# Kernel optimization log

Measured on AMD Instinct MI355X. Metric: run time of the kernel, lower is better.

## Reference

```python
import jax, jax.numpy as jnp
import numpy as np

B, NC, CN, K, DN = 2, 256, 256, 16, 64
G, HM, HS, HMOD, MOD_OUT = 8, 128, 128, 64, 5


def setup_inputs() -> dict:
    rng = np.random.default_rng(0)
    # per-neuron top-K neighbors within cell, excluding self, sorted (matches torch buffer build)
    scores = rng.random((NC, CN, CN)).astype(np.float32)
    ii = np.arange(CN)
    scores[:, ii, ii] = -np.inf
    conn = np.argpartition(-scores, K, axis=-1)[..., :K]
    conn = np.sort(conn, axis=-1).astype(np.int32)  # [NC, CN, K]

    key = jax.random.key(0)
    ks = jax.random.split(key, 12)
    n = lambda k, s, sc=1.0: jax.random.normal(k, s, jnp.float32) * sc
    return {
        'h': n(ks[0], (B, NC, CN, DN), 0.01),
        'w_conn': n(ks[1], (B, NC, CN, K), 0.1),
        'cell_context': n(ks[2], (B, NC, DN), 0.1),
        'neuron_id': n(ks[3], (NC, CN, DN), 0.02),
        'msg_w1': n(ks[4], (G, HM, 3 * DN), 0.05), 'msg_b1': jnp.zeros((G, HM)),
        'msg_w2': n(ks[5], (G, DN, HM), 0.005), 'msg_b2': jnp.zeros((G, DN)),
        'state_w1': n(ks[6], (G, HS, 3 * DN), 0.05), 'state_b1': jnp.zeros((G, HS)),
        'state_w2': n(ks[7], (G, DN, HS), 0.005), 'state_b2': jnp.zeros((G, DN)),
        'mod_w1': n(ks[8], (NC, 2 * DN, HMOD), 0.05), 'mod_b1': jnp.zeros((NC, HMOD)),
        'mod_w2': n(ks[9], (NC, HMOD, MOD_OUT), 0.0005), 'mod_b2': jnp.zeros((NC, MOD_OUT)),
        'conn_idx': jnp.asarray(conn),
        'cell_to_group': (jnp.arange(NC) % G).astype(jnp.int32),
    }


def reference(h, w_conn, cell_context, neuron_id,
              msg_w1, msg_b1, msg_w2, msg_b2,
              state_w1, state_b1, state_w2, state_b2,
              mod_w1, mod_b1, mod_w2, mod_b2,
              conn_idx, cell_to_group):
    nc = h.shape[1]
    cell_ix = jnp.arange(nc)[:, None, None]
    # gather K-neighbor states per neuron: [B, NC, CN, K, DN]
    nb = jax.vmap(lambda hb: hb[cell_ix, conn_idx])(h)
    # connection-weighted aggregation
    agg = jnp.einsum('bnck,bnckd->bncd', w_conn, nb)

    g = cell_to_group  # [NC]
    # grouped message MLP (2-layer), per-cell weights gathered from group table
    mfeat = jnp.concatenate([h, agg, jnp.broadcast_to(neuron_id[None], h.shape)], axis=-1)
    mh = jax.nn.gelu(jnp.einsum('bncf,nhf->bnch', mfeat, msg_w1[g]) + msg_b1[g][None, :, None, :])
    msg = jnp.einsum('bnch,ndh->bncd', mh, msg_w2[g]) + msg_b2[g][None, :, None, :]

    # grouped state MLP, residual update on h
    ctx = jnp.broadcast_to(cell_context[:, :, None, :], h.shape)
    sfeat = jnp.concatenate([h, msg, ctx], axis=-1)
    sh = jax.nn.gelu(jnp.einsum('bncf,nhf->bnch', sfeat, state_w1[g]) + state_b1[g][None, :, None, :])
    h_new = h + jnp.einsum('bnch,ndh->bncd', sh, state_w2[g]) + state_b2[g][None, :, None, :]

    # per-cell modulation MLP on pooled stats (h_mean || msg_mean)
    pooled = jnp.concatenate([h_new.mean(axis=2), msg.mean(axis=2)], axis=-1)  # [B, NC, 2DN]
    ph = jax.nn.gelu(jnp.einsum('bnf,nfh->bnh', pooled, mod_w1) + mod_b1[None])
    mod = jnp.einsum('bnh,nho->bno', ph, mod_w2) + mod_b2[None]
    return h_new, msg, mod
```

## Files before the change

### kernel.cpp

```cpp
#include <hip/hip_runtime.h>

#define B_   2
#define NC_  256
#define CN_  256
#define K_   16
#define DN_  64
#define G_   8
#define HM_  128
#define F3_  192

typedef unsigned short u16;
typedef short v8s __attribute__((ext_vector_type(8)));
typedef float v4f __attribute__((ext_vector_type(4)));

#define SMEM_BYTES 158336


__device__ __forceinline__ u16 f2b(float f) {
    unsigned v; __builtin_memcpy(&v, &f, 4);
    v = v + 0x7fffu + ((v >> 16) & 1u);
    return (u16)(v >> 16);
}
__device__ __forceinline__ v8s cvt8(const float* p) {
    float4 a = *(const float4*)p, b = *(const float4*)(p + 4);
    v8s r;
    r[0] = (short)f2b(a.x); r[1] = (short)f2b(a.y); r[2] = (short)f2b(a.z); r[3] = (short)f2b(a.w);
    r[4] = (short)f2b(b.x); r[5] = (short)f2b(b.y); r[6] = (short)f2b(b.z); r[7] = (short)f2b(b.w);
    return r;
}
__device__ __forceinline__ float gelu_t(float x) {
    float u = x * x;
    float t = 1.5957691216057308f * x * __builtin_fmaf(0.044715f, u, 1.0f);
    float e = __expf(-t);
    return x * __builtin_amdgcn_rcpf(1.0f + e);
}

__global__ __launch_bounds__(256) void cvt_w(
    const float* __restrict__ mw1, const float* __restrict__ mw2,
    const float* __restrict__ sw1, const float* __restrict__ sw2,
    u16* __restrict__ dst)
{
    int e = (blockIdx.x * 256 + threadIdx.x) * 4;
    const float* s; int off;
    if      (e < 196608) { s = mw1; off = e; }
    else if (e < 262144) { s = mw2; off = e - 196608; }
    else if (e < 458752) { s = sw1; off = e - 262144; }
    else                 { s = sw2; off = e - 458752; }
    float4 v = *(const float4*)(s + off);
    ushort4 o4;
    o4.x = f2b(v.x); o4.y = f2b(v.y); o4.z = f2b(v.z); o4.w = f2b(v.w);
    *(ushort4*)(dst + e) = o4;
}

__global__ __launch_bounds__(512) void mg_main(
    const float* __restrict__ h,    const float* __restrict__ wconn,
    const float* __restrict__ ctx,  const float* __restrict__ nid,
    const u16* __restrict__ mw1b,   const float* __restrict__ mb1,
    const u16* __restrict__ mw2b,   const float* __restrict__ mb2,
    const u16* __restrict__ sw1b,   const float* __restrict__ sb1,
    const u16* __restrict__ sw2b,   const float* __restrict__ sb2,
    const int* __restrict__ conn,   const int* __restrict__ c2g,
    const float* __restrict__ dw1,  const float* __restrict__ db1,
    const float* __restrict__ dw2,  const float* __restrict__ db2,
    float* __restrict__ outf)
{
    const int bn   = blockIdx.x;
    const int n    = bn & 255;
    const int tid  = threadIdx.x;
    const int wave = tid >> 6;
    const int lane = tid & 63;
    const int q    = lane >> 4;
    const int ln   = lane & 15;
    const int g    = c2g[n];

    extern __shared__ char smem[];
    u16*   hT   = (u16*)(smem);
    u16*   big  = (u16*)(smem + 34816);
    u16*   am   = (u16*)(smem + 104448);
    u16*   ctxl = (u16*)(smem + 141312);
    float* hsum = (float*)(smem + 141440);
    float* msum = (float*)(smem + 149632);
    float* pool = (float*)(smem + 157824);

    const size_t hbase = (size_t)bn * (CN_ * DN_);
    const size_t nbase = (size_t)n  * (CN_ * DN_);
    float* oH = outf + (size_t)bn * 16384;
    float* oM = outf + (size_t)8388608 + (size_t)bn * 16384;

    if (tid < 64) ctxl[tid] = f2b(ctx[(size_t)bn * DN_ + tid]);
    {
        const int row  = tid & 255;
        const int half = tid >> 8;
        const float* hrow = h + hbase + (size_t)row * DN_ + half * 32;
#pragma unroll
        for (int i = 0; i < 8; ++i) {
            float4 v = *(const float4*)(hrow + i * 4);
            int d0 = half * 32 + i * 4;
            hT[(d0 + 0) * 272 + row] = f2b(v.x);
            hT[(d0 + 1) * 272 + row] = f2b(v.y);
            hT[(d0 + 2) * 272 + row] = f2b(v.z);
            hT[(d0 + 3) * 272 + row] = f2b(v.w);
        }
    }
    __syncthreads();

    {
        const int sg   = wave >> 2;
        const int wl   = wave & 3;
        const int gtid = tid & 255;
        u16* wgg = (u16*)(smem + 34816 + sg * 34816);

        for (int s = 0; s < 4; s += 2) {
            const int st = s + sg;
#pragma unroll
            for (int i = 0; i < 9; ++i) {
                int idx = gtid + i * 256;
                if (idx < 2176) ((uint4*)wgg)[idx] = make_uint4(0u, 0u, 0u, 0u);
            }
            __syncthreads();
#pragma unroll
            for (int i = 0; i < 4; ++i) {
                int p  = i * 256 + gtid;
                int cl = p >> 4;
                int iv = conn[n * 4096 + st * 1024 + p];
                float wv = wconn[(size_t)bn * 4096 + st * 1024 + p];
                wgg[cl * 272 + iv] = f2b(wv);
            }
            __syncthreads();
            {
                v4f a0 = {0,0,0,0}, a1 = {0,0,0,0}, a2 = {0,0,0,0}, a3 = {0,0,0,0};
                const u16* arow = wgg + (wl * 16 + ln) * 272 + q * 8;
#pragma unroll
                for (int ks = 0; ks < 8; ++ks) {
                    v8s a   = *(const v8s*)(arow + ks * 32);
                    v8s bb0 = *(const v8s*)(hT + ( 0 + ln) * 272 + ks * 32 + q * 8);
                    v8s bb1 = *(const v8s*)(hT + (16 + ln) * 272 + ks * 32 + q * 8);
                    v8s bb2 = *(const v8s*)(hT + (32 + ln) * 272 + ks * 32 + q * 8);
                    v8s bb3 = *(const v8s*)(hT + (48 + ln) * 272 + ks * 32 + q * 8);
                    a0 = __builtin_amdgcn_mfma_f32_16x16x32_bf16(a, bb0, a0, 0, 0, 0);
                    a1 = __builtin_amdgcn_mfma_f32_16x16x32_bf16(a, bb1, a1, 0, 0, 0);
                    a2 = __builtin_amdgcn_mfma_f32_16x16x32_bf16(a, bb2, a2, 0, 0, 0);
                    a3 = __builtin_amdgcn_mfma_f32_16x16x32_bf16(a, bb3, a3, 0, 0, 0);
                }
                int crow = st * 64 + wl * 16 + q * 4;
#pragma unroll
                for (int r = 0; r < 4; ++r) {
                    am[(crow + r) * 72 +  0 + ln] = f2b(a0[r]);
                    am[(crow + r) * 72 + 16 + ln] = f2b(a1[r]);
                    am[(crow + r) * 72 + 32 + ln] = f2b(a2[r]);
                    am[(crow + r) * 72 + 48 + ln] = f2b(a3[r]);
                }
            }
            __syncthreads();
        }
    }

    const int cbase = wave * 32;

    {
        v8s afr[2][6];
#pragma unroll
        for (int mi = 0; mi < 2; ++mi) {
            int c = cbase + mi * 16 + ln;
            afr[mi][0] = cvt8(h + hbase + (size_t)c * 64 +  0 + q * 8);
            afr[mi][1] = cvt8(h + hbase + (size_t)c * 64 + 32 + q * 8);
            afr[mi][2] = *(const v8s*)(am + c * 72 +  0 + q * 8);
            afr[mi][3] = *(const v8s*)(am + c * 72 + 32 + q * 8);
            afr[mi][4] = cvt8(nid + nbase + (size_t)c * 64 +  0 + q * 8);
            afr[mi][5] = cvt8(nid + nbase + (size_t)c * 64 + 32 + q * 8);
        }
        float b1v[8];
#pragma unroll
        for (int nt = 0; nt < 8; ++nt) b1v[nt] = mb1[g * HM_ + nt * 16 + ln];
        const u16* w1g = mw1b + (size_t)g * HM_ * F3_;
#pragma unroll
        for (int nt = 0; nt < 8; ++nt) {
            v4f acc[2] = {{0,0,0,0},{0,0,0,0}};
#pragma unroll
            for (int ks = 0; ks < 6; ++ks) {
                v8s bf = *(const v8s*)(w1g + (nt * 16 + ln) * F3_ + ks * 32 + q * 8);
#pragma unroll
                for (int mi = 0; mi < 2; ++mi)
                    acc[mi] = __builtin_amdgcn_mfma_f32_16x16x32_bf16(afr[mi][ks], bf, acc[mi], 0, 0, 0);
            }
#pragma unroll
            for (int mi = 0; mi < 2; ++mi) {
                int c = cbase + mi * 16 + q * 4;
#pragma unroll
                for (int r = 0; r < 4; ++r)
                    big[(c + r) * 136 + nt * 16 + ln] = f2b(gelu_t(acc[mi][r] + b1v[nt]));
            }
        }
    }

    {
        v8s afr[2][4];
#pragma unroll
        for (int mi = 0; mi < 2; ++mi) {
            int c = cbase + mi * 16 + ln;
#pragma unroll
            for (int ks = 0; ks < 4; ++ks)
                afr[mi][ks] = *(const v8s*)(big + c * 136 + ks * 32 + q * 8);
        }
        const u16* w2g = mw2b + (size_t)g * DN_ * HM_;
        float mpart[4];
#pragma unroll
        for (int nt = 0; nt < 4; ++nt) {
            float bb = mb2[g * DN_ + nt * 16 + ln];
            v4f acc[2] = {{0,0,0,0},{0,0,0,0}};
#pragma unroll
            for (int ks = 0; ks < 4; ++ks) {
                v8s bf = *(const v8s*)(w2g + (nt * 16 + ln) * HM_ + ks * 32 + q * 8);
#pragma unroll
                for (int mi = 0; mi < 2; ++mi)
                    acc[mi] = __builtin_amdgcn_mfma_f32_16x16x32_bf16(afr[mi][ks], bf, acc[mi], 0, 0, 0);
            }
            float ms = 0.0f;
            int d = nt * 16 + ln;
#pragma unroll
            for (int mi = 0; mi < 2; ++mi) {
                int c = cbase + mi * 16 + q * 4;
#pragma unroll
                for (int r = 0; r < 4; ++r) {
                    float mv = acc[mi][r] + bb;
                    am[(c + r) * 72 + d] = f2b(mv);
                    oM[(size_t)(c + r) * 64 + d] = mv;
                    ms += mv;
                }
            }
            mpart[nt] = ms;
        }
#pragma unroll
        for (int nt = 0; nt < 4; ++nt)
            msum[(wave * 4 + q) * 64 + nt * 16 + ln] = mpart[nt];
    }

    {
        v8s cfr0 = *(const v8s*)(ctxl +  0 + q * 8);
        v8s cfr1 = *(const v8s*)(ctxl + 32 + q * 8);
        v8s afr[2][4];
#pragma unroll
        for (int mi = 0; mi < 2; ++mi) {
            int c = cbase + mi * 16 + ln;
            afr[mi][0] = cvt8(h + hbase + (size_t)c * 64 +  0 + q * 8);
            afr[mi][1] = cvt8(h + hbase + (size_t)c * 64 + 32 + q * 8);
            afr[mi][2] = *(const v8s*)(am + c * 72 +  0 + q * 8);
            afr[mi][3] = *(const v8s*)(am + c * 72 + 32 + q * 8);
        }
        float b1v[8];
#pragma unroll
        for (int nt = 0; nt < 8; ++nt) b1v[nt] = sb1[g * HM_ + nt * 16 + ln];
        const u16* w1g = sw1b + (size_t)g * HM_ * F3_;
#pragma unroll
        for (int nt = 0; nt < 8; ++nt) {
            v4f acc[2] = {{0,0,0,0},{0,0,0,0}};
#pragma unroll
            for (int ks = 0; ks < 4; ++ks) {
                v8s bf = *(const v8s*)(w1g + (nt * 16 + ln) * F3_ + ks * 32 + q * 8);
#pragma unroll
                for (int mi = 0; mi < 2; ++mi)
                    acc[mi] = __builtin_amdgcn_mfma_f32_16x16x32_bf16(afr[mi][ks], bf, acc[mi], 0, 0, 0);
            }
#pragma unroll
            for (int ks = 4; ks < 6; ++ks) {
                v8s bf = *(const v8s*)(w1g + (nt * 16 + ln) * F3_ + ks * 32 + q * 8);
                v8s aa = (ks == 4) ? cfr0 : cfr1;
#pragma unroll
                for (int mi = 0; mi < 2; ++mi)
                    acc[mi] = __builtin_amdgcn_mfma_f32_16x16x32_bf16(aa, bf, acc[mi], 0, 0, 0);
            }
#pragma unroll
            for (int mi = 0; mi < 2; ++mi) {
                int c = cbase + mi * 16 + q * 4;
#pragma unroll
                for (int r = 0; r < 4; ++r)
                    big[(c + r) * 136 + nt * 16 + ln] = f2b(gelu_t(acc[mi][r] + b1v[nt]));
            }
        }
    }

    {
        v8s afr[2][4];
#pragma unroll
        for (int mi = 0; mi < 2; ++mi) {
            int c = cbase + mi * 16 + ln;
#pragma unroll
            for (int ks = 0; ks < 4; ++ks)
                afr[mi][ks] = *(const v8s*)(big + c * 136 + ks * 32 + q * 8);
        }
        const u16* w2g = sw2b + (size_t)g * DN_ * HM_;
        float hpart[4];
#pragma unroll
        for (int nt = 0; nt < 4; ++nt) {
            float bb = sb2[g * DN_ + nt * 16 + ln];
            v4f acc[2] = {{0,0,0,0},{0,0,0,0}};
#pragma unroll
            for (int ks = 0; ks < 4; ++ks) {
                v8s bf = *(const v8s*)(w2g + (nt * 16 + ln) * HM_ + ks * 32 + q * 8);
#pragma unroll
                for (int mi = 0; mi < 2; ++mi)
                    acc[mi] = __builtin_amdgcn_mfma_f32_16x16x32_bf16(afr[mi][ks], bf, acc[mi], 0, 0, 0);
            }
            float hs = 0.0f;
            int d = nt * 16 + ln;
#pragma unroll
            for (int mi = 0; mi < 2; ++mi) {
                int c = cbase + mi * 16 + q * 4;
#pragma unroll
                for (int r = 0; r < 4; ++r) {
                    float hv = h[hbase + (size_t)(c + r) * 64 + d];
                    float hn = hv + acc[mi][r] + bb;
                    oH[(size_t)(c + r) * 64 + d] = hn;
                    hs += hn;
                }
            }
            hpart[nt] = hs;
        }
#pragma unroll
        for (int nt = 0; nt < 4; ++nt)
            hsum[(wave * 4 + q) * 64 + nt * 16 + ln] = hpart[nt];
    }
    __syncthreads();

    if (tid < 128) {
        int col = tid & 63;
        const float* src = (tid < 64) ? hsum : msum;
        float s = 0.0f;
#pragma unroll
        for (int i = 0; i < 32; ++i) s += src[i * 64 + col];
        pool[tid] = s * (1.0f / 256.0f);
    }
    __syncthreads();

    {
        const int col = tid & 63, fh = tid >> 6;
        const float* w1p = dw1 + ((size_t)n * 128 + fh * 16) * 64 + col;
        const float* pv  = pool + fh * 16;
        float acc = 0.0f;
#pragma unroll
        for (int f = 0; f < 16; ++f)
            acc = __builtin_fmaf(pv[f], w1p[(size_t)f * 64], acc);
        hsum[fh * 64 + col] = acc;
    }
    __syncthreads();

    if (tid < 64) {
        float a = db1[n * 64 + tid];
#pragma unroll
        for (int j = 0; j < 8; ++j) a += hsum[j * 64 + tid];
        float ph = gelu_t(a);
        float part[5];
#pragma unroll
        for (int o = 0; o < 5; ++o) part[o] = ph * dw2[((size_t)n * 64 + tid) * 5 + o];
#pragma unroll
        for (int off = 32; off > 0; off >>= 1)
#pragma unroll
            for (int o = 0; o < 5; ++o) part[o] += __shfl_down(part[o], off);
        if (tid == 0) {
#pragma unroll
            for (int o = 0; o < 5; ++o)
                outf[(size_t)16777216 + bn * 5 + o] = part[o] + db2[n * 5 + o];
        }
    }
}

extern "C" void kernel_launch(void* const* d_in, const int* in_sizes, int n_in,
                              void* d_out, int out_size, void* d_ws, size_t ws_size,
                              hipStream_t stream) {
    const float* h     = (const float*)d_in[0];
    const float* wconn = (const float*)d_in[1];
    const float* ctx   = (const float*)d_in[2];
    const float* nid   = (const float*)d_in[3];
    const float* mw1   = (const float*)d_in[4];
    const float* mb1   = (const float*)d_in[5];
    const float* mw2   = (const float*)d_in[6];
    const float* mb2   = (const float*)d_in[7];
    const float* sw1   = (const float*)d_in[8];
    const float* sb1   = (const float*)d_in[9];
    const float* sw2   = (const float*)d_in[10];
    const float* sb2   = (const float*)d_in[11];
    const float* dw1   = (const float*)d_in[12];
    const float* db1   = (const float*)d_in[13];
    const float* dw2   = (const float*)d_in[14];
    const float* db2   = (const float*)d_in[15];
    const int* conn    = (const int*)d_in[16];
    const int* c2g     = (const int*)d_in[17];
    float* outf  = (float*)d_out;
    u16*   wb    = (u16*)d_ws;

    hipFuncSetAttribute(reinterpret_cast<const void*>(&mg_main),
                        hipFuncAttributeMaxDynamicSharedMemorySize, SMEM_BYTES);

    cvt_w<<<512, 256, 0, stream>>>(mw1, mw2, sw1, sw2, wb);
    mg_main<<<512, 512, SMEM_BYTES, stream>>>(h, wconn, ctx, nid,
                                              wb,           mb1,
                                              wb + 196608,  mb2,
                                              wb + 262144,  sb1,
                                              wb + 458752,  sb2,
                                              conn, c2g,
                                              dw1, db1, dw2, db2,
                                              outf);
}
```

Baseline: 235.5 us.

## Split each cell across two blocks and gather neighbors directly instead of via MFMA

The main kernel now launches 1024 blocks of 256 threads, each covering half of a cell's neurons, with much smaller LDS so that two blocks fit per CU. The neighbor aggregation no longer builds a dense 256x256 scatter matrix for an MFMA. Instead each wave gathers bf16 h rows with readlane-broadcast indices and weights and accumulates with scalar FMAs. h is converted to bf16 once in LDS and reused for the MLP inputs. Pooled partial means go to workspace, and a new small kernel runs the modulation MLP, which adds a launch and a global round trip.

```diff
diff --git a/kernel.cpp b/kernel.cpp
--- a/kernel.cpp
+++ b/kernel.cpp
@@ -13,7 +13,7 @@
 typedef short v8s __attribute__((ext_vector_type(8)));
 typedef float v4f __attribute__((ext_vector_type(4)));
 
-#define SMEM_BYTES 158336
+#define SMEM_BYTES 63616
 
 
 __device__ __forceinline__ u16 f2b(float f) {
@@ -52,7 +52,7 @@
     *(ushort4*)(dst + e) = o4;
 }
 
-__global__ __launch_bounds__(512) void mg_main(
+__global__ __launch_bounds__(256, 2) void mg_main(
     const float* __restrict__ h,    const float* __restrict__ wconn,
     const float* __restrict__ ctx,  const float* __restrict__ nid,
     const u16* __restrict__ mw1b,   const float* __restrict__ mb1,
@@ -60,12 +60,13 @@
     const u16* __restrict__ sw1b,   const float* __restrict__ sb1,
     const u16* __restrict__ sw2b,   const float* __restrict__ sb2,
     const int* __restrict__ conn,   const int* __restrict__ c2g,
-    const float* __restrict__ dw1,  const float* __restrict__ db1,
-    const float* __restrict__ dw2,  const float* __restrict__ db2,
-    float* __restrict__ outf)
+    float* __restrict__ outf,       float* __restrict__ partial)
 {
-    const int bn   = blockIdx.x;
-    const int n    = bn & 255;
+    const int bx   = blockIdx.x;
+    const int bnc  = bx & 511;
+    const int half = bx >> 9;
+    const int r0   = half * 128;
+    const int n    = bnc & 255;
     const int tid  = threadIdx.x;
     const int wave = tid >> 6;
     const int lane = tid & 63;
@@ -74,133 +75,98 @@
     const int g    = c2g[n];
 
     extern __shared__ char smem[];
-    u16*   hT   = (u16*)(smem);
-    u16*   big  = (u16*)(smem + 34816);
-    u16*   am   = (u16*)(smem + 104448);
-    u16*   ctxl = (u16*)(smem + 141312);
-    float* hsum = (float*)(smem + 141440);
-    float* msum = (float*)(smem + 149632);
-    float* pool = (float*)(smem + 157824);
-
-    const size_t hbase = (size_t)bn * (CN_ * DN_);
-    const size_t nbase = (size_t)n  * (CN_ * DN_);
-    float* oH = outf + (size_t)bn * 16384;
-    float* oM = outf + (size_t)8388608 + (size_t)bn * 16384;
-
-    if (tid < 64) ctxl[tid] = f2b(ctx[(size_t)bn * DN_ + tid]);
-    {
-        const int row  = tid & 255;
-        const int half = tid >> 8;
-        const float* hrow = h + hbase + (size_t)row * DN_ + half * 32;
-#pragma unroll
-        for (int i = 0; i < 8; ++i) {
-            float4 v = *(const float4*)(hrow + i * 4);
-            int d0 = half * 32 + i * 4;
-            hT[(d0 + 0) * 272 + row] = f2b(v.x);
-            hT[(d0 + 1) * 272 + row] = f2b(v.y);
-            hT[(d0 + 2) * 272 + row] = f2b(v.z);
-            hT[(d0 + 3) * 272 + row] = f2b(v.w);
-        }
-    }
-    __syncthreads();
-
-    {
-        const int sg   = wave >> 2;
-        const int wl   = wave & 3;
-        const int gtid = tid & 255;
-        u16* wgg = (u16*)(smem + 34816 + sg * 34816);
-
-        for (int s = 0; s < 4; s += 2) {
-            const int st = s + sg;
-#pragma unroll
-            for (int i = 0; i < 9; ++i) {
-                int idx = gtid + i * 256;
-                if (idx < 2176) ((uint4*)wgg)[idx] = make_uint4(0u, 0u, 0u, 0u);
-            }
-            __syncthreads();
-#pragma unroll
-            for (int i = 0; i < 4; ++i) {
-                int p  = i * 256 + gtid;
-                int cl = p >> 4;
-                int iv = conn[n * 4096 + st * 1024 + p];
-                float wv = wconn[(size_t)bn * 4096 + st * 1024 + p];
-                wgg[cl * 272 + iv] = f2b(wv);
-            }
-            __syncthreads();
-            {
-                v4f a0 = {0,0,0,0}, a1 = {0,0,0,0}, a2 = {0,0,0,0}, a3 = {0,0,0,0};
-                const u16* arow = wgg + (wl * 16 + ln) * 272 + q * 8;
-#pragma unroll
-                for (int ks = 0; ks < 8; ++ks) {
-                    v8s a   = *(const v8s*)(arow + ks * 32);
-                    v8s bb0 = *(const v8s*)(hT + ( 0 + ln) * 272 + ks * 32 + q * 8);
-                    v8s bb1 = *(const v8s*)(hT + (16 + ln) * 272 + ks * 32 + q * 8);
-                    v8s bb2 = *(const v8s*)(hT + (32 + ln) * 272 + ks * 32 + q * 8);
-                    v8s bb3 = *(const v8s*)(hT + (48 + ln) * 272 + ks * 32 + q * 8);
-                    a0 = __builtin_amdgcn_mfma_f32_16x16x32_bf16(a, bb0, a0, 0, 0, 0);
-                    a1 = __builtin_amdgcn_mfma_f32_16x16x32_bf16(a, bb1, a1, 0, 0, 0);
-                    a2 = __builtin_amdgcn_mfma_f32_16x16x32_bf16(a, bb2, a2, 0, 0, 0);
-                    a3 = __builtin_amdgcn_mfma_f32_16x16x32_bf16(a, bb3, a3, 0, 0, 0);
-                }
-                int crow = st * 64 + wl * 16 + q * 4;
-#pragma unroll
-                for (int r = 0; r < 4; ++r) {
-                    am[(crow + r) * 72 +  0 + ln] = f2b(a0[r]);
-                    am[(crow + r) * 72 + 16 + ln] = f2b(a1[r]);
-                    am[(crow + r) * 72 + 32 + ln] = f2b(a2[r]);
-                    am[(crow + r) * 72 + 48 + ln] = f2b(a3[r]);
-                }
-            }
-            __syncthreads();
-        }
-    }
+    u16*   hbf  = (u16*)(smem);
+    u16*   mh   = (u16*)(smem);
+    u16*   am   = (u16*)(smem + 36864);
+    u16*   ctxl = (u16*)(smem + 55296);
+    float* hsum = (float*)(smem + 55424);
+    float* msum = (float*)(smem + 59520);
+
+    const size_t hbase = (size_t)bnc * (CN_ * DN_);
+    const size_t nbase = (size_t)n   * (CN_ * DN_);
+    float* oH = outf + (size_t)bnc * 16384;
+    float* oM = outf + (size_t)8388608 + (size_t)bnc * 16384;
+
+    if (tid < 64) ctxl[tid] = f2b(ctx[(size_t)bnc * DN_ + tid]);
+    {
+        const float* hrow = h + hbase + (size_t)tid * DN_;
+        u16* drow = hbf + tid * 72;
+#pragma unroll
+        for (int i = 0; i < 8; ++i)
+            *(v8s*)(drow + i * 8) = cvt8(hrow + i * 8);
+    }
+    __syncthreads();
 
     const int cbase = wave * 32;
 
     {
-        v8s afr[2][6];
+        const int kl = lane & 15;
+        const int* cp       = conn + n * 4096 + (size_t)(r0 + cbase) * 16;
+        const unsigned* wp  = (const unsigned*)(wconn + (size_t)bnc * 4096 + (size_t)(r0 + cbase) * 16);
+        int ivv      = cp[kl];
+        unsigned wvv = wp[kl];
+        for (int c = 0; c < 32; ++c) {
+            int ivn = 0; unsigned wvn = 0u;
+            if (c < 31) { ivn = cp[(c + 1) * 16 + kl]; wvn = wp[(c + 1) * 16 + kl]; }
+            float acc = 0.0f;
+#pragma unroll
+            for (int k = 0; k < 16; ++k) {
+                int iv = __builtin_amdgcn_readlane(ivv, k);
+                int wu = __builtin_amdgcn_readlane((int)wvv, k);
+                unsigned hu = (unsigned)hbf[iv * 72 + lane] << 16;
+                acc = __builtin_fmaf(__uint_as_float((unsigned)wu), __uint_as_float(hu), acc);
+            }
+            am[(cbase + c) * 72 + lane] = f2b(acc);
+            ivv = ivn; wvv = wvn;
+        }
+    }
+
+    v8s hfr[2][2], gfr[2][2], nfr[2][2];
+#pragma unroll
+    for (int mi = 0; mi < 2; ++mi) {
+        int c = cbase + mi * 16 + ln;
+        hfr[mi][0] = *(const v8s*)(hbf + (r0 + c) * 72 +  0 + q * 8);
+        hfr[mi][1] = *(const v8s*)(hbf + (r0 + c) * 72 + 32 + q * 8);
+        gfr[mi][0] = *(const v8s*)(am  + c * 72 +  0 + q * 8);
+        gfr[mi][1] = *(const v8s*)(am  + c * 72 + 32 + q * 8);
+        nfr[mi][0] = cvt8(nid + nbase + (size_t)(r0 + c) * 64 +  0 + q * 8);
+        nfr[mi][1] = cvt8(nid + nbase + (size_t)(r0 + c) * 64 + 32 + q * 8);
+    }
+    __syncthreads();
+
+    {
+        v8s afr[6] = {hfr[0][0], hfr[0][1], gfr[0][0], gfr[0][1], nfr[0][0], nfr[0][1]};
+        v8s afr1[6] = {hfr[1][0], hfr[1][1], gfr[1][0], gfr[1][1], nfr[1][0], nfr[1][1]};
+        float b1v[8];
+#pragma unroll
+        for (int nt = 0; nt < 8; ++nt) b1v[nt] = mb1[g * HM_ + nt * 16 + ln];
+        const u16* w1g = mw1b + (size_t)g * HM_ * F3_;
+#pragma unroll
+        for (int nt = 0; nt < 8; ++nt) {
+            v4f acc0 = {0,0,0,0}, acc1 = {0,0,0,0};
+#pragma unroll
+            for (int ks = 0; ks < 6; ++ks) {
+                v8s bf = *(const v8s*)(w1g + (nt * 16 + ln) * F3_ + ks * 32 + q * 8);
+                acc0 = __builtin_amdgcn_mfma_f32_16x16x32_bf16(afr[ks],  bf, acc0, 0, 0, 0);
+                acc1 = __builtin_amdgcn_mfma_f32_16x16x32_bf16(afr1[ks], bf, acc1, 0, 0, 0);
+            }
+            int c0 = cbase + q * 4, c1 = cbase + 16 + q * 4;
+#pragma unroll
+            for (int r = 0; r < 4; ++r) {
+                mh[(c0 + r) * 136 + nt * 16 + ln] = f2b(gelu_t(acc0[r] + b1v[nt]));
+                mh[(c1 + r) * 136 + nt * 16 + ln] = f2b(gelu_t(acc1[r] + b1v[nt]));
+            }
+        }
+    }
+
+    {
+        v8s afr[2][4];
 #pragma unroll
         for (int mi = 0; mi < 2; ++mi) {
             int c = cbase + mi * 16 + ln;
-            afr[mi][0] = cvt8(h + hbase + (size_t)c * 64 +  0 + q * 8);
-            afr[mi][1] = cvt8(h + hbase + (size_t)c * 64 + 32 + q * 8);
-            afr[mi][2] = *(const v8s*)(am + c * 72 +  0 + q * 8);
-            afr[mi][3] = *(const v8s*)(am + c * 72 + 32 + q * 8);
-            afr[mi][4] = cvt8(nid + nbase + (size_t)c * 64 +  0 + q * 8);
-            afr[mi][5] = cvt8(nid + nbase + (size_t)c * 64 + 32 + q * 8);
-        }
-        float b1v[8];
-#pragma unroll
-        for (int nt = 0; nt < 8; ++nt) b1v[nt] = mb1[g * HM_ + nt * 16 + ln];
-        const u16* w1g = mw1b + (size_t)g * HM_ * F3_;
-#pragma unroll
-        for (int nt = 0; nt < 8; ++nt) {
-            v4f acc[2] = {{0,0,0,0},{0,0,0,0}};
-#pragma unroll
-            for (int ks = 0; ks < 6; ++ks) {
-                v8s bf = *(const v8s*)(w1g + (nt * 16 + ln) * F3_ + ks * 32 + q * 8);
-#pragma unroll
-                for (int mi = 0; mi < 2; ++mi)
-                    acc[mi] = __builtin_amdgcn_mfma_f32_16x16x32_bf16(afr[mi][ks], bf, acc[mi], 0, 0, 0);
-            }
-#pragma unroll
-            for (int mi = 0; mi < 2; ++mi) {
-                int c = cbase + mi * 16 + q * 4;
-#pragma unroll
-                for (int r = 0; r < 4; ++r)
-                    big[(c + r) * 136 + nt * 16 + ln] = f2b(gelu_t(acc[mi][r] + b1v[nt]));
-            }
-        }
-    }
-
-    {
-        v8s afr[2][4];
-#pragma unroll
-        for (int mi = 0; mi < 2; ++mi) {
-            int c = cbase + mi * 16 + ln;
 #pragma unroll
             for (int ks = 0; ks < 4; ++ks)
-                afr[mi][ks] = *(const v8s*)(big + c * 136 + ks * 32 + q * 8);
+                afr[mi][ks] = *(const v8s*)(mh + c * 136 + ks * 32 + q * 8);
         }
         const u16* w2g = mw2b + (size_t)g * DN_ * HM_;
         float mpart[4];
@@ -224,7 +190,7 @@
                 for (int r = 0; r < 4; ++r) {
                     float mv = acc[mi][r] + bb;
                     am[(c + r) * 72 + d] = f2b(mv);
-                    oM[(size_t)(c + r) * 64 + d] = mv;
+                    oM[(size_t)(r0 + c + r) * 64 + d] = mv;
                     ms += mv;
                 }
             }
@@ -242,8 +208,8 @@
 #pragma unroll
         for (int mi = 0; mi < 2; ++mi) {
             int c = cbase + mi * 16 + ln;
-            afr[mi][0] = cvt8(h + hbase + (size_t)c * 64 +  0 + q * 8);
-            afr[mi][1] = cvt8(h + hbase + (size_t)c * 64 + 32 + q * 8);
+            afr[mi][0] = hfr[mi][0];
+            afr[mi][1] = hfr[mi][1];
             afr[mi][2] = *(const v8s*)(am + c * 72 +  0 + q * 8);
             afr[mi][3] = *(const v8s*)(am + c * 72 + 32 + q * 8);
         }
@@ -274,7 +240,7 @@
                 int c = cbase + mi * 16 + q * 4;
 #pragma unroll
                 for (int r = 0; r < 4; ++r)
-                    big[(c + r) * 136 + nt * 16 + ln] = f2b(gelu_t(acc[mi][r] + b1v[nt]));
+                    mh[(c + r) * 136 + nt * 16 + ln] = f2b(gelu_t(acc[mi][r] + b1v[nt]));
             }
         }
     }
@@ -286,7 +252,7 @@
             int c = cbase + mi * 16 + ln;
 #pragma unroll
             for (int ks = 0; ks < 4; ++ks)
-                afr[mi][ks] = *(const v8s*)(big + c * 136 + ks * 32 + q * 8);
+                afr[mi][ks] = *(const v8s*)(mh + c * 136 + ks * 32 + q * 8);
         }
         const u16* w2g = sw2b + (size_t)g * DN_ * HM_;
         float hpart[4];
@@ -308,9 +274,9 @@
                 int c = cbase + mi * 16 + q * 4;
 #pragma unroll
                 for (int r = 0; r < 4; ++r) {
-                    float hv = h[hbase + (size_t)(c + r) * 64 + d];
+                    float hv = h[hbase + (size_t)(r0 + c + r) * 64 + d];
                     float hn = hv + acc[mi][r] + bb;
-                    oH[(size_t)(c + r) * 64 + d] = hn;
+                    oH[(size_t)(r0 + c + r) * 64 + d] = hn;
                     hs += hn;
                 }
             }
@@ -327,39 +293,46 @@
         const float* src = (tid < 64) ? hsum : msum;
         float s = 0.0f;
 #pragma unroll
-        for (int i = 0; i < 32; ++i) s += src[i * 64 + col];
-        pool[tid] = s * (1.0f / 256.0f);
-    }
-    __syncthreads();
-
-    {
-        const int col = tid & 63, fh = tid >> 6;
-        const float* w1p = dw1 + ((size_t)n * 128 + fh * 16) * 64 + col;
-        const float* pv  = pool + fh * 16;
+        for (int i = 0; i < 16; ++i) s += src[i * 64 + col];
+        partial[(size_t)(bnc * 2 + half) * 128 + (tid < 64 ? col : 64 + col)] = s * (1.0f / 256.0f);
+    }
+}
+
+__global__ __launch_bounds__(256) void mg_mod(
+    const float* __restrict__ w1, const float* __restrict__ b1,
+    const float* __restrict__ w2, const float* __restrict__ b2,
+    const float* __restrict__ partial, float* __restrict__ outf)
+{
+    __shared__ float pool[128];
+    __shared__ float ph4[4][64];
+    const int bnc = blockIdx.x, n = bnc & 255, t = threadIdx.x;
+    if (t < 128)
+        pool[t] = partial[(size_t)(bnc * 2) * 128 + t] + partial[(size_t)(bnc * 2 + 1) * 128 + t];
+    __syncthreads();
+    {
+        const int col = t & 63, fh = t >> 6;
+        const float* w1p = w1 + ((size_t)n * 128 + fh * 32) * 64 + col;
         float acc = 0.0f;
 #pragma unroll
-        for (int f = 0; f < 16; ++f)
-            acc = __builtin_fmaf(pv[f], w1p[(size_t)f * 64], acc);
-        hsum[fh * 64 + col] = acc;
-    }
-    __syncthreads();
-
-    if (tid < 64) {
-        float a = db1[n * 64 + tid];
-#pragma unroll
-        for (int j = 0; j < 8; ++j) a += hsum[j * 64 + tid];
+        for (int i = 0; i < 32; ++i)
+            acc = __builtin_fmaf(pool[fh * 32 + i], w1p[(size_t)i * 64], acc);
+        ph4[fh][col] = acc;
+    }
+    __syncthreads();
+    if (t < 64) {
+        float a  = ph4[0][t] + ph4[1][t] + ph4[2][t] + ph4[3][t] + b1[n * 64 + t];
         float ph = gelu_t(a);
-        float part[5];
-#pragma unroll
-        for (int o = 0; o < 5; ++o) part[o] = ph * dw2[((size_t)n * 64 + tid) * 5 + o];
+        float part5[5];
+#pragma unroll
+        for (int o = 0; o < 5; ++o) part5[o] = ph * w2[((size_t)n * 64 + t) * 5 + o];
 #pragma unroll
         for (int off = 32; off > 0; off >>= 1)
 #pragma unroll
-            for (int o = 0; o < 5; ++o) part[o] += __shfl_down(part[o], off);
-        if (tid == 0) {
+            for (int o = 0; o < 5; ++o) part5[o] += __shfl_down(part5[o], off);
+        if (t == 0) {
 #pragma unroll
             for (int o = 0; o < 5; ++o)
-                outf[(size_t)16777216 + bn * 5 + o] = part[o] + db2[n * 5 + o];
+                outf[(size_t)16777216 + bnc * 5 + o] = part5[o] + b2[n * 5 + o];
         }
     }
 }
@@ -385,19 +358,19 @@
     const float* db2   = (const float*)d_in[15];
     const int* conn    = (const int*)d_in[16];
     const int* c2g     = (const int*)d_in[17];
-    float* outf  = (float*)d_out;
-    u16*   wb    = (u16*)d_ws;
+    float* outf   = (float*)d_out;
+    u16*   wb     = (u16*)d_ws;
+    float* partial = (float*)((char*)d_ws + 1048576);
 
     hipFuncSetAttribute(reinterpret_cast<const void*>(&mg_main),
                         hipFuncAttributeMaxDynamicSharedMemorySize, SMEM_BYTES);
 
     cvt_w<<<512, 256, 0, stream>>>(mw1, mw2, sw1, sw2, wb);
-    mg_main<<<512, 512, SMEM_BYTES, stream>>>(h, wconn, ctx, nid,
-                                              wb,           mb1,
-                                              wb + 196608,  mb2,
-                                              wb + 262144,  sb1,
-                                              wb + 458752,  sb2,
-                                              conn, c2g,
-                                              dw1, db1, dw2, db2,
-                                              outf);
-}
+    mg_main<<<1024, 256, SMEM_BYTES, stream>>>(h, wconn, ctx, nid,
+                                               wb,           mb1,
+                                               wb + 196608,  mb2,
+                                               wb + 262144,  sb1,
+                                               wb + 458752,  sb2,
+                                               conn, c2g, outf, partial);
+    mg_mod<<<512, 256, 0, stream>>>(dw1, db1, dw2, db2, partial, outf);
+}
```

After: 239.1 us. No clear change (+1.5%).
